# Kernel tuning notes

Hardware: AMD Instinct MI355X
Metric: run time of the kernel (lower is better)

Reference implementation:

```python
import jax, jax.numpy as jnp
import numpy as np

K = 10          # hardcoded in module (self.K = 10)
H = 26          # neighbors per query point in this run
PAD_H = 28      # layer_ind2neighbor[layer_ind=0]
KP_EXTENT = 1.2 # linear-influence extent


def setup_inputs() -> dict:
    key = jax.random.key(0)
    ks = jax.random.split(key, 6)
    N, Ns, Cin, Cout = 65536, 65536, 64, 128
    q_pts = jax.random.normal(ks[0], (N, 3), jnp.float32)
    s_pts = jax.random.normal(ks[1], (Ns, 3), jnp.float32)
    neighb_inds = jax.random.randint(ks[2], (N, H), 0, Ns)
    x = jax.random.normal(ks[3], (Ns, Cin), jnp.float32)
    # kernel_points_generator: Linear(PAD_H*3 -> K*3)
    gen_W = jax.random.normal(ks[4], (K * 3, PAD_H * 3), jnp.float32) * (1.0 / np.sqrt(PAD_H * 3))
    gen_b = jnp.zeros((K * 3,), jnp.float32)
    # KPConv weights: [K, in, out] (kaiming_uniform in torch; scaled normal here)
    weights = jax.random.normal(ks[5], (K, Cin, Cout), jnp.float32) * (1.0 / np.sqrt(Cin))
    return {"q_pts": q_pts, "s_pts": s_pts, "x": x,
            "gen_W": gen_W, "gen_b": gen_b, "weights": weights,
            "neighb_inds": neighb_inds}


def _kpconv(q_pts, s_pts, x, gen_W, gen_b, weights, neighb_inds):
    N = q_pts.shape[0]
    # shadow support point far away (index Ns)
    s_pad = jnp.concatenate([s_pts, jnp.full((1, 3), 1e6, s_pts.dtype)], axis=0)
    neighbors = s_pad[neighb_inds] - q_pts[:, None, :]                          # [N,H,3]
    # generative kernel points: pad neighbor list with -1 up to PAD_H, run linear
    padded = jnp.concatenate(
        [neighbors, jnp.full((N, PAD_H - H, 3), -1.0, neighbors.dtype)], axis=1)
    kp = (padded.reshape(N, -1) @ gen_W.T + gen_b).reshape(N, 1, K, 3)          # [N,1,K,3]
    diff = neighbors[:, :, None, :] - kp                                        # [N,H,K,3]
    sq_d = jnp.sum(diff * diff, axis=3)                                         # [N,H,K]
    # KP_influence == 'linear'
    all_w = jnp.maximum(1.0 - jnp.sqrt(sq_d) / KP_EXTENT, 0.0)
    all_w = jnp.swapaxes(all_w, 1, 2)                                           # [N,K,H]
    # shadow feature row (zeros) at index Ns
    x_pad = jnp.concatenate([x, jnp.zeros((1, x.shape[1]), x.dtype)], axis=0)
    neighb_x = x_pad[neighb_inds]                                               # [N,H,Cin]
    weighted = jnp.einsum('nkh,nhi->nki', all_w, neighb_x)                      # [N,K,Cin]
    return jnp.einsum('nki,kio->no', weighted, weights)                         # [N,Cout]


def reference(q_pts, s_pts, x, gen_W, gen_b, weights, neighb_inds):
    return _kpconv(q_pts, s_pts, x, gen_W, gen_b, weights, neighb_inds)
```

## Files before the change

kernel.cpp:

```cpp
#include <hip/hip_runtime.h>
#include <stdint.h>

#define N_Q   65536
#define N_S   65536
#define NB_H  26
#define PAD_H 28
#define KP    10
#define CIN   64
#define COUT  128
#define MT    16

typedef unsigned short u16x4  __attribute__((ext_vector_type(4)));
typedef unsigned short u16x8  __attribute__((ext_vector_type(8)));
typedef float          f32x4  __attribute__((ext_vector_type(4)));
typedef __bf16         bf16x8 __attribute__((ext_vector_type(8)));

static __device__ __forceinline__ unsigned short f2bf(float f) {
  unsigned int u = __float_as_uint(f);
  u += 0x7fffu + ((u >> 16) & 1u);
  return (unsigned short)(u >> 16);
}
static __device__ __forceinline__ float bf2f(unsigned short h) {
  return __uint_as_float(((unsigned int)h) << 16);
}

__global__ void cvt_x_kernel(const float* __restrict__ x,
                             unsigned short* __restrict__ xb) {
  long t = (long)blockIdx.x * blockDim.x + threadIdx.x;
  long off = t * 8;
  if (off >= (long)(N_S + 1) * CIN) return;
  u16x8 o;
  if (off < (long)N_S * CIN) {
    f32x4 a = *(const f32x4*)(x + off);
    f32x4 b = *(const f32x4*)(x + off + 4);
    o[0] = f2bf(a[0]); o[1] = f2bf(a[1]); o[2] = f2bf(a[2]); o[3] = f2bf(a[3]);
    o[4] = f2bf(b[0]); o[5] = f2bf(b[1]); o[6] = f2bf(b[2]); o[7] = f2bf(b[3]);
  } else {
    o = (u16x8)0;
  }
  *(u16x8*)(xb + off) = o;
}

__global__ void pack_w_kernel(const float* __restrict__ w,
                              unsigned short* __restrict__ bp) {
  int t = blockIdx.x * blockDim.x + threadIdx.x;
  if (t >= 8 * 20 * 64) return;
  int lane = t & 63;
  int frag = t >> 6;
  int ks = frag % 20;
  int ct = frag / 20;
  int row0 = ks * 32 + (lane >> 4) * 8;
  int col  = ct * 16 + (lane & 15);
  u16x8 o;
  #pragma unroll
  for (int j = 0; j < 8; ++j) o[j] = f2bf(w[(row0 + j) * COUT + col]);
  *(u16x8*)(bp + (long)t * 8) = o;
}

__global__ void __launch_bounds__(256, 4)
kpconv_main(const float* __restrict__ q_pts, const float* __restrict__ s_pts,
            const float* __restrict__ gen_W, const float* __restrict__ gen_b,
            const int* __restrict__ inds, const unsigned short* __restrict__ xb,
            const unsigned short* __restrict__ bp, float* __restrict__ out) {

  __shared__ int   sh_ind[MT][NB_H];
  __shared__ float sh_aw[MT][KP * NB_H];
  __shared__ __align__(16) char pool[MT * 648 * 2];

  float* sh_nbr = (float*)pool;
  float* sh_kp  = (float*)(pool + MT * NB_H * 3 * 4);
  unsigned short* sh_w = (unsigned short*)pool;

  const int tid  = threadIdx.x;
  const int base = blockIdx.x * MT;

  for (int p = tid; p < MT * NB_H; p += 256) {
    int m = p / NB_H, h = p % NB_H;
    int n = base + m;
    int ind = inds[n * NB_H + h];
    sh_ind[m][h] = ind;
    float sx, sy, sz;
    if ((unsigned)ind < (unsigned)N_S) {
      sx = s_pts[ind * 3 + 0]; sy = s_pts[ind * 3 + 1]; sz = s_pts[ind * 3 + 2];
    } else {
      sx = 1e6f; sy = 1e6f; sz = 1e6f;
    }
    sh_nbr[(m * NB_H + h) * 3 + 0] = sx - q_pts[n * 3 + 0];
    sh_nbr[(m * NB_H + h) * 3 + 1] = sy - q_pts[n * 3 + 1];
    sh_nbr[(m * NB_H + h) * 3 + 2] = sz - q_pts[n * 3 + 2];
  }
  __syncthreads();

  for (int p = tid; p < MT * KP * 3; p += 256) {
    int m = p / (KP * 3), r = p % (KP * 3);
    const float* Wr = gen_W + r * (PAD_H * 3);
    float acc = gen_b[r];
    #pragma unroll
    for (int c = NB_H * 3; c < PAD_H * 3; ++c) acc -= Wr[c];
    for (int h = 0; h < NB_H; ++h) {
      acc += Wr[h * 3 + 0] * sh_nbr[(m * NB_H + h) * 3 + 0]
           + Wr[h * 3 + 1] * sh_nbr[(m * NB_H + h) * 3 + 1]
           + Wr[h * 3 + 2] * sh_nbr[(m * NB_H + h) * 3 + 2];
    }
    sh_kp[m * KP * 3 + r] = acc;
  }
  __syncthreads();

  for (int p = tid; p < MT * KP * NB_H; p += 256) {
    int m = p / (KP * NB_H);
    int r = p - m * (KP * NB_H);
    int k = r / NB_H, h = r % NB_H;
    float dx = sh_nbr[(m * NB_H + h) * 3 + 0] - sh_kp[m * KP * 3 + k * 3 + 0];
    float dy = sh_nbr[(m * NB_H + h) * 3 + 1] - sh_kp[m * KP * 3 + k * 3 + 1];
    float dz = sh_nbr[(m * NB_H + h) * 3 + 2] - sh_kp[m * KP * 3 + k * 3 + 2];
    float d  = sqrtf(dx * dx + dy * dy + dz * dz);
    sh_aw[m][k * NB_H + h] = fmaxf(1.0f - d * (1.0f / 1.2f), 0.0f);
  }
  __syncthreads();

  {
    const int m  = tid >> 4;
    const int i0 = (tid & 15) * 4;
    float acc[KP][4];
    #pragma unroll
    for (int k = 0; k < KP; ++k)
      #pragma unroll
      for (int j = 0; j < 4; ++j) acc[k][j] = 0.0f;

    int ind0 = sh_ind[m][0];
    int ind1 = sh_ind[m][1];
    u16x4 xv0 = *(const u16x4*)(xb + (long)ind0 * CIN + i0);
    u16x4 xv1 = *(const u16x4*)(xb + (long)ind1 * CIN + i0);

    for (int h = 0; h < NB_H; ++h) {
      u16x4 xc = xv0;
      xv0 = xv1;
      int hp = h + 2; if (hp > NB_H - 1) hp = NB_H - 1;
      int indp = sh_ind[m][hp];
      xv1 = *(const u16x4*)(xb + (long)indp * CIN + i0);

      float xf0 = bf2f(xc[0]), xf1 = bf2f(xc[1]);
      float xf2 = bf2f(xc[2]), xf3 = bf2f(xc[3]);
      #pragma unroll
      for (int k = 0; k < KP; ++k) {
        float w = sh_aw[m][k * NB_H + h];
        acc[k][0] = fmaf(w, xf0, acc[k][0]);
        acc[k][1] = fmaf(w, xf1, acc[k][1]);
        acc[k][2] = fmaf(w, xf2, acc[k][2]);
        acc[k][3] = fmaf(w, xf3, acc[k][3]);
      }
    }
    __syncthreads();
    #pragma unroll
    for (int k = 0; k < KP; ++k) {
      u16x4 o;
      #pragma unroll
      for (int j = 0; j < 4; ++j) o[j] = f2bf(acc[k][j]);
      *(u16x4*)&sh_w[m * 648 + k * CIN + i0] = o;
    }
  }
  __syncthreads();

  {
    const int wave = tid >> 6;
    const int lane = tid & 63;
    const int arow = lane & 15;
    const int ak   = (lane >> 4) * 8;
    const int ct0  = wave * 2, ct1 = ct0 + 1;
    f32x4 acc0 = {0.f, 0.f, 0.f, 0.f}, acc1 = {0.f, 0.f, 0.f, 0.f};
    for (int ks = 0; ks < 20; ++ks) {
      u16x8 au  = *(const u16x8*)&sh_w[arow * 648 + ks * 32 + ak];
      u16x8 b0u = *(const u16x8*)(bp + (long)((ct0 * 20 + ks) * 64 + lane) * 8);
      u16x8 b1u = *(const u16x8*)(bp + (long)((ct1 * 20 + ks) * 64 + lane) * 8);
      bf16x8 a  = __builtin_bit_cast(bf16x8, au);
      bf16x8 b0 = __builtin_bit_cast(bf16x8, b0u);
      bf16x8 b1 = __builtin_bit_cast(bf16x8, b1u);
      acc0 = __builtin_amdgcn_mfma_f32_16x16x32_bf16(a, b0, acc0, 0, 0, 0);
      acc1 = __builtin_amdgcn_mfma_f32_16x16x32_bf16(a, b1, acc1, 0, 0, 0);
    }
    const int col   = lane & 15;
    const int rbase = (lane >> 4) * 4;
    #pragma unroll
    for (int r = 0; r < 4; ++r) {
      out[(long)(base + rbase + r) * COUT + ct0 * 16 + col] = acc0[r];
      out[(long)(base + rbase + r) * COUT + ct1 * 16 + col] = acc1[r];
    }
  }
}

extern "C" void kernel_launch(void* const* d_in, const int* in_sizes, int n_in,
                              void* d_out, int out_size, void* d_ws, size_t ws_size,
                              hipStream_t stream) {
  const float* q_pts = (const float*)d_in[0];
  const float* s_pts = (const float*)d_in[1];
  const float* x     = (const float*)d_in[2];
  const float* gen_W = (const float*)d_in[3];
  const float* gen_b = (const float*)d_in[4];
  const float* wts   = (const float*)d_in[5];
  const int*   inds  = (const int*)d_in[6];
  float* out = (float*)d_out;

  unsigned short* xb = (unsigned short*)d_ws;
  unsigned short* bp = xb + (size_t)(N_S + 1) * CIN;

  long cvt_elems = (long)(N_S + 1) * CIN / 8;
  cvt_x_kernel<<<(int)((cvt_elems + 255) / 256), 256, 0, stream>>>(x, xb);
  pack_w_kernel<<<40, 256, 0, stream>>>(wts, bp);
  kpconv_main<<<N_Q / MT, 256, 0, stream>>>(q_pts, s_pts, gen_W, gen_b,
                                            inds, xb, bp, out);
}
```

Before: 196.7 us.

## Fuse prep kernels, deepen gather prefetch to 13 rows, transpose weight layout

```diff
diff --git a/kernel.cpp b/kernel.cpp
--- a/kernel.cpp
+++ b/kernel.cpp
@@ -15,6 +15,9 @@
 typedef float          f32x4  __attribute__((ext_vector_type(4)));
 typedef __bf16         bf16x8 __attribute__((ext_vector_type(8)));
 
+#define CVT_BLOCKS 2049
+#define PACK_BLOCKS 40
+
 static __device__ __forceinline__ unsigned short f2bf(float f) {
   unsigned int u = __float_as_uint(f);
   u += 0x7fffu + ((u >> 16) & 1u);
@@ -24,37 +27,38 @@
   return __uint_as_float(((unsigned int)h) << 16);
 }
 
-__global__ void cvt_x_kernel(const float* __restrict__ x,
-                             unsigned short* __restrict__ xb) {
-  long t = (long)blockIdx.x * blockDim.x + threadIdx.x;
-  long off = t * 8;
-  if (off >= (long)(N_S + 1) * CIN) return;
-  u16x8 o;
-  if (off < (long)N_S * CIN) {
-    f32x4 a = *(const f32x4*)(x + off);
-    f32x4 b = *(const f32x4*)(x + off + 4);
-    o[0] = f2bf(a[0]); o[1] = f2bf(a[1]); o[2] = f2bf(a[2]); o[3] = f2bf(a[3]);
-    o[4] = f2bf(b[0]); o[5] = f2bf(b[1]); o[6] = f2bf(b[2]); o[7] = f2bf(b[3]);
+__global__ void prep_kernel(const float* __restrict__ x,
+                            const float* __restrict__ w,
+                            unsigned short* __restrict__ xb,
+                            unsigned short* __restrict__ bp) {
+  if (blockIdx.x < CVT_BLOCKS) {
+    long t = (long)blockIdx.x * blockDim.x + threadIdx.x;
+    long off = t * 8;
+    if (off >= (long)(N_S + 1) * CIN) return;
+    u16x8 o;
+    if (off < (long)N_S * CIN) {
+      f32x4 a = *(const f32x4*)(x + off);
+      f32x4 b = *(const f32x4*)(x + off + 4);
+      o[0] = f2bf(a[0]); o[1] = f2bf(a[1]); o[2] = f2bf(a[2]); o[3] = f2bf(a[3]);
+      o[4] = f2bf(b[0]); o[5] = f2bf(b[1]); o[6] = f2bf(b[2]); o[7] = f2bf(b[3]);
+    } else {
+      o = (u16x8)0;
+    }
+    *(u16x8*)(xb + off) = o;
   } else {
-    o = (u16x8)0;
-  }
-  *(u16x8*)(xb + off) = o;
-}
-
-__global__ void pack_w_kernel(const float* __restrict__ w,
-                              unsigned short* __restrict__ bp) {
-  int t = blockIdx.x * blockDim.x + threadIdx.x;
-  if (t >= 8 * 20 * 64) return;
-  int lane = t & 63;
-  int frag = t >> 6;
-  int ks = frag % 20;
-  int ct = frag / 20;
-  int row0 = ks * 32 + (lane >> 4) * 8;
-  int col  = ct * 16 + (lane & 15);
-  u16x8 o;
-  #pragma unroll
-  for (int j = 0; j < 8; ++j) o[j] = f2bf(w[(row0 + j) * COUT + col]);
-  *(u16x8*)(bp + (long)t * 8) = o;
+    int t = (blockIdx.x - CVT_BLOCKS) * blockDim.x + threadIdx.x;
+    if (t >= 8 * 20 * 64) return;
+    int lane = t & 63;
+    int frag = t >> 6;
+    int ks = frag % 20;
+    int ct = frag / 20;
+    int row0 = ks * 32 + (lane >> 4) * 8;
+    int col  = ct * 16 + (lane & 15);
+    u16x8 o;
+    #pragma unroll
+    for (int j = 0; j < 8; ++j) o[j] = f2bf(w[(row0 + j) * COUT + col]);
+    *(u16x8*)(bp + (long)t * 8) = o;
+  }
 }
 
 __global__ void __launch_bounds__(256, 4)
@@ -64,7 +68,7 @@
             const unsigned short* __restrict__ bp, float* __restrict__ out) {
 
   __shared__ int   sh_ind[MT][NB_H];
-  __shared__ float sh_aw[MT][KP * NB_H];
+  __shared__ float sh_aw[MT][NB_H * KP];
   __shared__ __align__(16) char pool[MT * 648 * 2];
 
   float* sh_nbr = (float*)pool;
@@ -114,7 +118,7 @@
     float dy = sh_nbr[(m * NB_H + h) * 3 + 1] - sh_kp[m * KP * 3 + k * 3 + 1];
     float dz = sh_nbr[(m * NB_H + h) * 3 + 2] - sh_kp[m * KP * 3 + k * 3 + 2];
     float d  = sqrtf(dx * dx + dy * dy + dz * dz);
-    sh_aw[m][k * NB_H + h] = fmaxf(1.0f - d * (1.0f / 1.2f), 0.0f);
+    sh_aw[m][h * KP + k] = fmaxf(1.0f - d * (1.0f / 1.2f), 0.0f);
   }
   __syncthreads();
 
@@ -127,23 +131,36 @@
       #pragma unroll
       for (int j = 0; j < 4; ++j) acc[k][j] = 0.0f;
 
-    int ind0 = sh_ind[m][0];
-    int ind1 = sh_ind[m][1];
-    u16x4 xv0 = *(const u16x4*)(xb + (long)ind0 * CIN + i0);
-    u16x4 xv1 = *(const u16x4*)(xb + (long)ind1 * CIN + i0);
-
-    for (int h = 0; h < NB_H; ++h) {
-      u16x4 xc = xv0;
-      xv0 = xv1;
-      int hp = h + 2; if (hp > NB_H - 1) hp = NB_H - 1;
-      int indp = sh_ind[m][hp];
-      xv1 = *(const u16x4*)(xb + (long)indp * CIN + i0);
-
+    u16x4 xr[13];
+    #pragma unroll
+    for (int h = 0; h < 13; ++h)
+      xr[h] = *(const u16x4*)(xb + (long)sh_ind[m][h] * CIN + i0);
+
+    #pragma unroll
+    for (int h = 0; h < 13; ++h) {
+      u16x4 xc = xr[h];
+      xr[h] = *(const u16x4*)(xb + (long)sh_ind[m][h + 13] * CIN + i0);
       float xf0 = bf2f(xc[0]), xf1 = bf2f(xc[1]);
       float xf2 = bf2f(xc[2]), xf3 = bf2f(xc[3]);
+      const float* wrow = &sh_aw[m][h * KP];
       #pragma unroll
       for (int k = 0; k < KP; ++k) {
-        float w = sh_aw[m][k * NB_H + h];
+        float w = wrow[k];
+        acc[k][0] = fmaf(w, xf0, acc[k][0]);
+        acc[k][1] = fmaf(w, xf1, acc[k][1]);
+        acc[k][2] = fmaf(w, xf2, acc[k][2]);
+        acc[k][3] = fmaf(w, xf3, acc[k][3]);
+      }
+    }
+    #pragma unroll
+    for (int h = 0; h < 13; ++h) {
+      u16x4 xc = xr[h];
+      float xf0 = bf2f(xc[0]), xf1 = bf2f(xc[1]);
+      float xf2 = bf2f(xc[2]), xf3 = bf2f(xc[3]);
+      const float* wrow = &sh_aw[m][(h + 13) * KP];
+      #pragma unroll
+      for (int k = 0; k < KP; ++k) {
+        float w = wrow[k];
         acc[k][0] = fmaf(w, xf0, acc[k][0]);
         acc[k][1] = fmaf(w, xf1, acc[k][1]);
         acc[k][2] = fmaf(w, xf2, acc[k][2]);
@@ -203,9 +220,7 @@
   unsigned short* xb = (unsigned short*)d_ws;
   unsigned short* bp = xb + (size_t)(N_S + 1) * CIN;
 
-  long cvt_elems = (long)(N_S + 1) * CIN / 8;
-  cvt_x_kernel<<<(int)((cvt_elems + 255) / 256), 256, 0, stream>>>(x, xb);
-  pack_w_kernel<<<40, 256, 0, stream>>>(wts, bp);
+  prep_kernel<<<CVT_BLOCKS + PACK_BLOCKS, 256, 0, stream>>>(x, wts, xb, bp);
   kpconv_main<<<N_Q / MT, 256, 0, stream>>>(q_pts, s_pts, gen_W, gen_b,
                                             inds, xb, bp, out);
 }
```

After: 221.4 us. 1.13x slower.
